# Kernel tuning notes

Measured on AMD Instinct MI355X. Metric: run time of the kernel, lower is better.

The kernel has to match this reference:

```python
import jax, jax.numpy as jnp
import numpy as np

# Sampled 2-layer GraphSAGE sizes (ogbn-products-like, fanouts [25, 10], batch 4096)
N0, N1, N2 = 1_000_000, 40_960, 4_096   # source nodes per hop / targets
E1, E2 = 1_024_000, 40_960              # edges per hop
IN_C, HID, OUT = 100, 256, 47


def setup_inputs() -> dict:
    key = jax.random.key(0)
    ks = jax.random.split(key, 10)
    x = jax.random.normal(ks[0], (N0, IN_C), jnp.float32)
    src1 = jax.random.randint(ks[1], (E1,), 0, N0, dtype=jnp.int64)
    dst1 = jax.random.randint(ks[2], (E1,), 0, N1, dtype=jnp.int64)
    src2 = jax.random.randint(ks[3], (E2,), 0, N1, dtype=jnp.int64)
    dst2 = jax.random.randint(ks[4], (E2,), 0, N2, dtype=jnp.int64)
    s1 = 1.0 / np.sqrt(IN_C)
    s2 = 1.0 / np.sqrt(HID)
    W1l = jax.random.uniform(ks[5], (IN_C, HID), jnp.float32, -s1, s1)
    W1r = jax.random.uniform(ks[6], (IN_C, HID), jnp.float32, -s1, s1)
    b1l = jnp.zeros((HID,), jnp.float32)
    W2l = jax.random.uniform(ks[7], (HID, OUT), jnp.float32, -s2, s2)
    W2r = jax.random.uniform(ks[8], (HID, OUT), jnp.float32, -s2, s2)
    b2l = jnp.zeros((OUT,), jnp.float32)
    return {"x": x, "W1l": W1l, "b1l": b1l, "W1r": W1r,
            "W2l": W2l, "b2l": b2l, "W2r": W2r,
            "src1": src1, "dst1": dst1, "src2": src2, "dst2": dst2}


def _sage_conv(x_src, x_dst, src, dst, Wl, bl, Wr, num_dst):
    # PyG SAGEConv (aggr='mean'): lin_l(mean_j x_j) + lin_r(x_target)
    msg = x_src[src]                                            # [E, C] gather
    agg = jax.ops.segment_sum(msg, dst, num_segments=num_dst)   # [num_dst, C]
    cnt = jax.ops.segment_sum(jnp.ones((src.shape[0], 1), x_src.dtype), dst,
                              num_segments=num_dst)
    agg = agg / jnp.maximum(cnt, 1.0)                           # mean (0 for isolated)
    return agg @ Wl + bl + x_dst @ Wr


def reference(x, W1l, b1l, W1r, W2l, b2l, W2r, src1, dst1, src2, dst2):
    # layer 1: bipartite (N0 -> N1)
    h = _sage_conv(x, x[:N1], src1, dst1, W1l, b1l, W1r, N1)
    h = jax.nn.relu(h)  # dropout is identity in eval mode
    # layer 2: bipartite (N1 -> N2)
    out = _sage_conv(h, h[:N2], src2, dst2, W2l, b2l, W2r, N2)
    return jax.nn.log_softmax(out, axis=-1)
```

## Files before the change

### kernel.cpp

```cpp
#include <hip/hip_runtime.h>
#include <math.h>

#define N0 1000000
#define N1 40960
#define N2 4096
#define E1 1024000
#define E2 40960
#define IN_C 100
#define HID 256
#define OUT_C 47
#define S1 128
#define S2 64

__global__ __launch_bounds__(256) void build_kernel(
    const int* __restrict__ src1, const int* __restrict__ dst1,
    const int* __restrict__ src2, const int* __restrict__ dst2,
    int* __restrict__ deg1, int* __restrict__ ell1,
    int* __restrict__ deg2, int* __restrict__ ell2) {
    int gid = blockIdx.x * 256 + threadIdx.x;
    if (gid < E1 / 2) {
        int2 s = ((const int2*)src1)[gid];
        int2 d = ((const int2*)dst1)[gid];
        int slot0 = atomicAdd(&deg1[d.x], 1);
        if (slot0 < S1) ell1[d.x * S1 + slot0] = s.x;
        int slot1 = atomicAdd(&deg1[d.y], 1);
        if (slot1 < S1) ell1[d.y * S1 + slot1] = s.y;
    } else {
        int p = gid - E1 / 2;
        int2 s = ((const int2*)src2)[p];
        int2 d = ((const int2*)dst2)[p];
        int slot0 = atomicAdd(&deg2[d.x], 1);
        if (slot0 < S2) ell2[d.x * S2 + slot0] = s.x;
        int slot1 = atomicAdd(&deg2[d.y], 1);
        if (slot1 < S2) ell2[d.y * S2 + slot1] = s.y;
    }
}

__global__ __launch_bounds__(256) void agg1_kernel(
    const float* __restrict__ x, const int* __restrict__ ell1,
    const int* __restrict__ deg1, float* __restrict__ aggm1) {
    int d = (blockIdx.x << 2) + (threadIdx.x >> 6);
    int lane = threadIdx.x & 63;
    int l2 = (lane < 50) ? lane : 49;
    int nd = deg1[d];
    int n = (nd < S1) ? nd : S1;
    const int* rp = ell1 + d * S1;

    float x0 = 0.f, y0 = 0.f, x1 = 0.f, y1 = 0.f;
    float x2 = 0.f, y2 = 0.f, x3 = 0.f, y3 = 0.f;
    int e = 0;
    for (; e + 7 < n; e += 8) {
        int s0 = rp[e],     s1 = rp[e + 1], s2 = rp[e + 2], s3 = rp[e + 3];
        int s4 = rp[e + 4], s5 = rp[e + 5], s6 = rp[e + 6], s7 = rp[e + 7];
        float2 v0 = ((const float2*)(x + s0 * IN_C))[l2];
        float2 v1 = ((const float2*)(x + s1 * IN_C))[l2];
        float2 v2 = ((const float2*)(x + s2 * IN_C))[l2];
        float2 v3 = ((const float2*)(x + s3 * IN_C))[l2];
        float2 v4 = ((const float2*)(x + s4 * IN_C))[l2];
        float2 v5 = ((const float2*)(x + s5 * IN_C))[l2];
        float2 v6 = ((const float2*)(x + s6 * IN_C))[l2];
        float2 v7 = ((const float2*)(x + s7 * IN_C))[l2];
        x0 += v0.x + v4.x; y0 += v0.y + v4.y;
        x1 += v1.x + v5.x; y1 += v1.y + v5.y;
        x2 += v2.x + v6.x; y2 += v2.y + v6.y;
        x3 += v3.x + v7.x; y3 += v3.y + v7.y;
    }
    for (; e + 1 < n; e += 2) {
        int s0 = rp[e], s1 = rp[e + 1];
        float2 v0 = ((const float2*)(x + s0 * IN_C))[l2];
        float2 v1 = ((const float2*)(x + s1 * IN_C))[l2];
        x0 += v0.x; y0 += v0.y;
        x1 += v1.x; y1 += v1.y;
    }
    if (e < n) {
        float2 v0 = ((const float2*)(x + rp[e] * IN_C))[l2];
        x0 += v0.x; y0 += v0.y;
    }
    float sx = (x0 + x1) + (x2 + x3);
    float sy = (y0 + y1) + (y2 + y3);
    float inv = 1.0f / (float)(nd > 0 ? nd : 1);
    if (lane < 50) {
        float2 o = {sx * inv, sy * inv};
        ((float2*)(aggm1 + d * IN_C))[lane] = o;
    }
}

__global__ __launch_bounds__(256) void gemm1_kernel(
    const float* __restrict__ aggm1, const float* __restrict__ x,
    const float* __restrict__ W1l, const float* __restrict__ b1l,
    const float* __restrict__ W1r, float* __restrict__ h) {
    __shared__ float axs[32][2 * IN_C];
    int tid = threadIdx.x;
    int i0 = blockIdx.x * 32;
    for (int idx = tid; idx < 32 * IN_C; idx += 256) {
        int r = idx / IN_C;
        int k = idx - r * IN_C;
        int row = i0 + r;
        axs[r][2 * k]     = aggm1[row * IN_C + k];
        axs[r][2 * k + 1] = x[row * IN_C + k];
    }
    __syncthreads();

    int jq = tid & 63;
    int rgrp = tid >> 6;
    int j4 = jq * 4;
    const float4* wl = (const float4*)(W1l + j4);
    const float4* wr = (const float4*)(W1r + j4);
    const float4* ax4 = (const float4*)(&axs[rgrp * 8][0]);

    float acc[8][4];
    #pragma unroll
    for (int r = 0; r < 8; ++r)
        #pragma unroll
        for (int c = 0; c < 4; ++c) acc[r][c] = 0.f;

    for (int k = 0; k < IN_C; k += 2) {
        float4 wl0 = wl[k * 64];
        float4 wr0 = wr[k * 64];
        float4 wl1 = wl[(k + 1) * 64];
        float4 wr1 = wr[(k + 1) * 64];
        int kh = k >> 1;
        #pragma unroll
        for (int r = 0; r < 8; ++r) {
            float4 v = ax4[r * 50 + kh];
            acc[r][0] += v.x * wl0.x + v.y * wr0.x + v.z * wl1.x + v.w * wr1.x;
            acc[r][1] += v.x * wl0.y + v.y * wr0.y + v.z * wl1.y + v.w * wr1.y;
            acc[r][2] += v.x * wl0.z + v.y * wr0.z + v.z * wl1.z + v.w * wr1.z;
            acc[r][3] += v.x * wl0.w + v.y * wr0.w + v.z * wl1.w + v.w * wr1.w;
        }
    }

    float4 b = *(const float4*)(b1l + j4);
    #pragma unroll
    for (int r = 0; r < 8; ++r) {
        int row = i0 + rgrp * 8 + r;
        float4 o;
        o.x = fmaxf(acc[r][0] + b.x, 0.f);
        o.y = fmaxf(acc[r][1] + b.y, 0.f);
        o.z = fmaxf(acc[r][2] + b.z, 0.f);
        o.w = fmaxf(acc[r][3] + b.w, 0.f);
        *(float4*)(h + row * HID + j4) = o;
    }
}

__global__ __launch_bounds__(256) void l2_fused_kernel(
    const float* __restrict__ h, const int* __restrict__ ell2,
    const int* __restrict__ deg2,
    const float* __restrict__ W2l, const float* __restrict__ b2l,
    const float* __restrict__ W2r, float* __restrict__ out) {
    __shared__ float sa[4][HID];
    __shared__ float sh_[4][HID];
    int w = threadIdx.x >> 6;
    int lane = threadIdx.x & 63;
    int row = (blockIdx.x << 2) + w;

    int nd = deg2[row];
    int n = (nd < S2) ? nd : S2;
    const int* rp = ell2 + row * S2;
    float4 acc4 = {0.f, 0.f, 0.f, 0.f};
    int e = 0;
    for (; e + 1 < n; e += 2) {
        int s0 = rp[e], s1 = rp[e + 1];
        float4 v0 = ((const float4*)(h + s0 * HID))[lane];
        float4 v1 = ((const float4*)(h + s1 * HID))[lane];
        acc4.x += v0.x + v1.x; acc4.y += v0.y + v1.y;
        acc4.z += v0.z + v1.z; acc4.w += v0.w + v1.w;
    }
    if (e < n) {
        int s0 = rp[e];
        float4 v0 = ((const float4*)(h + s0 * HID))[lane];
        acc4.x += v0.x; acc4.y += v0.y; acc4.z += v0.z; acc4.w += v0.w;
    }
    float inv = 1.0f / (float)(nd > 0 ? nd : 1);
    float4 am = {acc4.x * inv, acc4.y * inv, acc4.z * inv, acc4.w * inv};
    ((float4*)&sa[w][0])[lane] = am;
    ((float4*)&sh_[w][0])[lane] = ((const float4*)(h + row * HID))[lane];
    __syncthreads();

    int j = lane;
    int jj = (j < OUT_C) ? j : (OUT_C - 1);
    float acc = 0.f;
    for (int k = 0; k < HID; k += 4) {
        float4 av = *(const float4*)&sa[w][k];
        float4 hv = *(const float4*)&sh_[w][k];
        acc += av.x * W2l[(k + 0) * OUT_C + jj] + hv.x * W2r[(k + 0) * OUT_C + jj];
        acc += av.y * W2l[(k + 1) * OUT_C + jj] + hv.y * W2r[(k + 1) * OUT_C + jj];
        acc += av.z * W2l[(k + 2) * OUT_C + jj] + hv.z * W2r[(k + 2) * OUT_C + jj];
        acc += av.w * W2l[(k + 3) * OUT_C + jj] + hv.w * W2r[(k + 3) * OUT_C + jj];
    }
    float v = acc + b2l[jj];
    float vm = (j < OUT_C) ? v : -__builtin_huge_valf();
    #pragma unroll
    for (int s = 32; s > 0; s >>= 1) vm = fmaxf(vm, __shfl_xor(vm, s));
    float ex = (j < OUT_C) ? __expf(v - vm) : 0.f;
    #pragma unroll
    for (int s = 32; s > 0; s >>= 1) ex += __shfl_xor(ex, s);
    if (j < OUT_C) out[row * OUT_C + j] = v - vm - __logf(ex);
}

extern "C" void kernel_launch(void* const* d_in, const int* in_sizes, int n_in,
                              void* d_out, int out_size, void* d_ws, size_t ws_size,
                              hipStream_t stream) {
    const float* x   = (const float*)d_in[0];
    const float* W1l = (const float*)d_in[1];
    const float* b1l = (const float*)d_in[2];
    const float* W1r = (const float*)d_in[3];
    const float* W2l = (const float*)d_in[4];
    const float* b2l = (const float*)d_in[5];
    const float* W2r = (const float*)d_in[6];
    const int* src1  = (const int*)d_in[7];
    const int* dst1  = (const int*)d_in[8];
    const int* src2  = (const int*)d_in[9];
    const int* dst2  = (const int*)d_in[10];
    float* out = (float*)d_out;

    char* ws = (char*)d_ws;
    size_t off = 0;
    auto alloc = [&](size_t bytes) {
        off = (off + 255) & ~(size_t)255;
        void* p = ws + off;
        off += bytes;
        return p;
    };

    int* deg1 = (int*)alloc(N1 * sizeof(int));
    int* deg2 = (int*)alloc(N2 * sizeof(int));
    int* ell1 = (int*)alloc((size_t)N1 * S1 * sizeof(int));
    int* ell2 = (int*)alloc((size_t)N2 * S2 * sizeof(int));
    float* aggm1 = (float*)alloc((size_t)N1 * IN_C * sizeof(float));
    float* h     = (float*)alloc((size_t)N1 * HID * sizeof(float));

    hipMemsetAsync(deg1, 0, (N1 + N2) * sizeof(int), stream);

    build_kernel<<<(E1 / 2 + E2 / 2) / 256, 256, 0, stream>>>(
        src1, dst1, src2, dst2, deg1, ell1, deg2, ell2);
    agg1_kernel<<<N1 / 4, 256, 0, stream>>>(x, ell1, deg1, aggm1);
    gemm1_kernel<<<N1 / 32, 256, 0, stream>>>(aggm1, x, W1l, b1l, W1r, h);
    l2_fused_kernel<<<N2 / 4, 256, 0, stream>>>(h, ell2, deg2, W2l, b2l, W2r, out);
}
```

Before: 710.1 us.

## Move layer-1 GEMM to bf16 MFMA with pre-packed weight fragments

Replaces the fp32 FMA layer-1 GEMM with bf16 MFMA 16x16x32 instructions. The concatenated [agg|x] tile is converted to bf16 in LDS, and W1l/W1r are packed into MFMA B-fragment layout by extra blocks added to the build kernel. This is meant to cut the compute cost of the 40960x200x256 GEMM. It lowers precision to bf16 inputs and adds a small packing pass, and the output stores become scattered scalar writes instead of float4 writes.

```diff
diff --git a/kernel.cpp b/kernel.cpp
--- a/kernel.cpp
+++ b/kernel.cpp
@@ -11,12 +11,46 @@
 #define OUT_C 47
 #define S1 128
 #define S2 64
-
+#define KCAT 224
+#define KSTEPS 7
+#define LDSTR 232
+
+typedef __attribute__((ext_vector_type(8))) short short8;
+typedef __attribute__((ext_vector_type(4))) float float4v;
+
+__device__ inline unsigned short f2bf(float f) {
+    union { float f; unsigned u; } v; v.f = f;
+    unsigned r = v.u + 0x7FFF + ((v.u >> 16) & 1);
+    return (unsigned short)(r >> 16);
+}
+
+#define EDGE_BLKS ((E1 / 2 + E2 / 2) / 256)
+#define PACK_BLKS 28
 __global__ __launch_bounds__(256) void build_kernel(
     const int* __restrict__ src1, const int* __restrict__ dst1,
     const int* __restrict__ src2, const int* __restrict__ dst2,
     int* __restrict__ deg1, int* __restrict__ ell1,
-    int* __restrict__ deg2, int* __restrict__ ell2) {
+    int* __restrict__ deg2, int* __restrict__ ell2,
+    const float* __restrict__ W1l, const float* __restrict__ W1r,
+    unsigned short* __restrict__ packedW) {
+    if (blockIdx.x >= EDGE_BLKS) {
+        int t = (blockIdx.x - EDGE_BLKS) * 256 + threadIdx.x;
+        int nt = t / 448;
+        int rem = t - nt * 448;
+        int ks = rem >> 6;
+        int lane = rem & 63;
+        int n = nt * 16 + (lane & 15);
+        int kbase = ks * 32 + (lane >> 4) * 8;
+        unsigned short* wp = packedW + (size_t)(nt * 7 + ks) * 512 + lane * 8;
+        #pragma unroll
+        for (int j = 0; j < 8; ++j) {
+            int k = kbase + j;
+            float v = (k < 100) ? W1l[k * HID + n]
+                    : (k < 200) ? W1r[(k - 100) * HID + n] : 0.f;
+            wp[j] = f2bf(v);
+        }
+        return;
+    }
     int gid = blockIdx.x * 256 + threadIdx.x;
     if (gid < E1 / 2) {
         int2 s = ((const int2*)src1)[gid];
@@ -87,59 +121,74 @@
 
 __global__ __launch_bounds__(256) void gemm1_kernel(
     const float* __restrict__ aggm1, const float* __restrict__ x,
-    const float* __restrict__ W1l, const float* __restrict__ b1l,
-    const float* __restrict__ W1r, float* __restrict__ h) {
-    __shared__ float axs[32][2 * IN_C];
+    const unsigned short* __restrict__ packedW, const float* __restrict__ b1l,
+    float* __restrict__ h) {
+    __shared__ short As[32 * LDSTR];
     int tid = threadIdx.x;
     int i0 = blockIdx.x * 32;
-    for (int idx = tid; idx < 32 * IN_C; idx += 256) {
-        int r = idx / IN_C;
-        int k = idx - r * IN_C;
-        int row = i0 + r;
-        axs[r][2 * k]     = aggm1[row * IN_C + k];
-        axs[r][2 * k + 1] = x[row * IN_C + k];
+
+    const float2* ag2 = (const float2*)(aggm1 + (size_t)i0 * IN_C);
+    for (int idx = tid; idx < 32 * 50; idx += 256) {
+        int r = idx / 50;
+        int p = idx - r * 50;
+        float2 v = ag2[idx];
+        short2 o = {(short)f2bf(v.x), (short)f2bf(v.y)};
+        *(short2*)(As + r * LDSTR + 2 * p) = o;
+    }
+    const float2* xs2 = (const float2*)(x + (size_t)i0 * IN_C);
+    for (int idx = tid; idx < 32 * 50; idx += 256) {
+        int r = idx / 50;
+        int p = idx - r * 50;
+        float2 v = xs2[idx];
+        short2 o = {(short)f2bf(v.x), (short)f2bf(v.y)};
+        *(short2*)(As + r * LDSTR + 100 + 2 * p) = o;
+    }
+    for (int idx = tid; idx < 32 * 12; idx += 256) {
+        int r = idx / 12;
+        int p = idx - r * 12;
+        short2 z = {0, 0};
+        *(short2*)(As + r * LDSTR + 200 + 2 * p) = z;
     }
     __syncthreads();
 
-    int jq = tid & 63;
-    int rgrp = tid >> 6;
-    int j4 = jq * 4;
-    const float4* wl = (const float4*)(W1l + j4);
-    const float4* wr = (const float4*)(W1r + j4);
-    const float4* ax4 = (const float4*)(&axs[rgrp * 8][0]);
-
-    float acc[8][4];
-    #pragma unroll
-    for (int r = 0; r < 8; ++r)
-        #pragma unroll
-        for (int c = 0; c < 4; ++c) acc[r][c] = 0.f;
-
-    for (int k = 0; k < IN_C; k += 2) {
-        float4 wl0 = wl[k * 64];
-        float4 wr0 = wr[k * 64];
-        float4 wl1 = wl[(k + 1) * 64];
-        float4 wr1 = wr[(k + 1) * 64];
-        int kh = k >> 1;
-        #pragma unroll
-        for (int r = 0; r < 8; ++r) {
-            float4 v = ax4[r * 50 + kh];
-            acc[r][0] += v.x * wl0.x + v.y * wr0.x + v.z * wl1.x + v.w * wr1.x;
-            acc[r][1] += v.x * wl0.y + v.y * wr0.y + v.z * wl1.y + v.w * wr1.y;
-            acc[r][2] += v.x * wl0.z + v.y * wr0.z + v.z * wl1.z + v.w * wr1.z;
-            acc[r][3] += v.x * wl0.w + v.y * wr0.w + v.z * wl1.w + v.w * wr1.w;
+    int lane = tid & 63;
+    int w = tid >> 6;
+    int quad = lane >> 4;
+    int m = lane & 15;
+
+    float4v acc[2][4];
+    #pragma unroll
+    for (int rt = 0; rt < 2; ++rt)
+        #pragma unroll
+        for (int c = 0; c < 4; ++c) acc[rt][c] = (float4v){0.f, 0.f, 0.f, 0.f};
+
+    #pragma unroll
+    for (int ks = 0; ks < KSTEPS; ++ks) {
+        int ko = ks * 32 + quad * 8;
+        short8 a0 = *(const short8*)(As + (0 * 16 + m) * LDSTR + ko);
+        short8 a1 = *(const short8*)(As + (1 * 16 + m) * LDSTR + ko);
+        #pragma unroll
+        for (int c = 0; c < 4; ++c) {
+            int nt = w * 4 + c;
+            short8 b = *(const short8*)(packedW + (size_t)(nt * 7 + ks) * 512 + lane * 8);
+            acc[0][c] = __builtin_amdgcn_mfma_f32_16x16x32_bf16(a0, b, acc[0][c], 0, 0, 0);
+            acc[1][c] = __builtin_amdgcn_mfma_f32_16x16x32_bf16(a1, b, acc[1][c], 0, 0, 0);
         }
     }
 
-    float4 b = *(const float4*)(b1l + j4);
-    #pragma unroll
-    for (int r = 0; r < 8; ++r) {
-        int row = i0 + rgrp * 8 + r;
-        float4 o;
-        o.x = fmaxf(acc[r][0] + b.x, 0.f);
-        o.y = fmaxf(acc[r][1] + b.y, 0.f);
-        o.z = fmaxf(acc[r][2] + b.z, 0.f);
-        o.w = fmaxf(acc[r][3] + b.w, 0.f);
-        *(float4*)(h + row * HID + j4) = o;
+    #pragma unroll
+    for (int c = 0; c < 4; ++c) {
+        int col = (w * 4 + c) * 16 + m;
+        float bv = b1l[col];
+        #pragma unroll
+        for (int rt = 0; rt < 2; ++rt) {
+            int rbase = i0 + rt * 16 + quad * 4;
+            #pragma unroll
+            for (int reg = 0; reg < 4; ++reg) {
+                float v = acc[rt][c][reg] + bv;
+                h[(size_t)(rbase + reg) * HID + col] = fmaxf(v, 0.f);
+            }
+        }
     }
 }
 
@@ -229,12 +278,13 @@
     int* ell2 = (int*)alloc((size_t)N2 * S2 * sizeof(int));
     float* aggm1 = (float*)alloc((size_t)N1 * IN_C * sizeof(float));
     float* h     = (float*)alloc((size_t)N1 * HID * sizeof(float));
+    unsigned short* packedW = (unsigned short*)alloc((size_t)16 * 7 * 512 * sizeof(unsigned short));
 
     hipMemsetAsync(deg1, 0, (N1 + N2) * sizeof(int), stream);
 
-    build_kernel<<<(E1 / 2 + E2 / 2) / 256, 256, 0, stream>>>(
-        src1, dst1, src2, dst2, deg1, ell1, deg2, ell2);
+    build_kernel<<<EDGE_BLKS + PACK_BLKS, 256, 0, stream>>>(
+        src1, dst1, src2, dst2, deg1, ell1, deg2, ell2, W1l, W1r, packedW);
     agg1_kernel<<<N1 / 4, 256, 0, stream>>>(x, ell1, deg1, aggm1);
-    gemm1_kernel<<<N1 / 32, 256, 0, stream>>>(aggm1, x, W1l, b1l, W1r, h);
+    gemm1_kernel<<<N1 / 32, 256, 0, stream>>>(aggm1, x, packedW, b1l, h);
     l2_fused_kernel<<<N2 / 4, 256, 0, stream>>>(h, ell2, deg2, W2l, b2l, W2r, out);
 }
```

Result: faster. 670.3 us (-5.6%).
